# Kernel tuning notes

Hardware: AMD Instinct MI355X
Metric: run time of the kernel (lower is better)

## Reference

```python
import jax, jax.numpy as jnp
import numpy as np

J = 16384
D = 2048

def setup_inputs() -> dict:
    key = jax.random.key(0)
    embeddings = jax.random.normal(key, (J, D), dtype=jnp.float32)
    return {"embeddings": embeddings}

def reference(embeddings) -> jnp.ndarray:
    J_, d = embeddings.shape
    # position indices j=1..J, feature indices k=1..d (as in the torch loop)
    j = jnp.arange(1, J_ + 1, dtype=embeddings.dtype)  # [J]
    k = jnp.arange(1, d + 1, dtype=embeddings.dtype)   # [d]
    a = 1.0 - j / J_            # [J]
    b = 1.0 - 2.0 * j / J_      # [J]
    # L[j,k] = (1 - j/J) - (k/d)*(1 - 2j/J)
    L = a[:, None] - (k / d)[None, :] * b[:, None]  # [J, d]
    return jnp.sum(L * embeddings, axis=0)  # [d]
```

## Files before the change

### kernel.cpp

```cpp
#include <hip/hip_runtime.h>


constexpr int D_COLS = 2048;
constexpr int J_ROWS = 16384;
constexpr int T1  = 512;
constexpr int NB1 = 1024;
constexpr int RPB = J_ROWS / NB1;

__global__ __launch_bounds__(T1, 8) void pe_stage1(const float* __restrict__ E,
                                                   float* __restrict__ ws) {
    const int tid  = threadIdx.x;
    const int col0 = tid * 4;
    const int b    = blockIdx.x;
    const int row0 = b * RPB;
    const float invJ = 1.0f / (float)J_ROWS;
    const float invD = 1.0f / (float)D_COLS;
    const float c0 = (float)(col0 + 1) * invD;
    const float c1 = (float)(col0 + 2) * invD;
    const float c2 = (float)(col0 + 3) * invD;
    const float c3 = (float)(col0 + 4) * invD;

    const float* base = E + (size_t)row0 * D_COLS + col0;

    float4 acc = make_float4(0.f, 0.f, 0.f, 0.f);
    #pragma unroll 1
    for (int it = 0; it < RPB / 4; ++it) {
        const int r = it * 4;
        const float4 e0 = *reinterpret_cast<const float4*>(base + (size_t)(r + 0) * D_COLS);
        const float4 e1 = *reinterpret_cast<const float4*>(base + (size_t)(r + 1) * D_COLS);
        const float4 e2 = *reinterpret_cast<const float4*>(base + (size_t)(r + 2) * D_COLS);
        const float4 e3 = *reinterpret_cast<const float4*>(base + (size_t)(r + 3) * D_COLS);

        const float j0 = (float)(row0 + r + 1);
        const float j1 = j0 + 1.0f, j2 = j0 + 2.0f, j3 = j0 + 3.0f;
        const float a0 = fmaf(-j0, invJ, 1.0f), bb0 = fmaf(-2.f * j0, invJ, 1.0f);
        const float a1 = fmaf(-j1, invJ, 1.0f), bb1 = fmaf(-2.f * j1, invJ, 1.0f);
        const float a2 = fmaf(-j2, invJ, 1.0f), bb2 = fmaf(-2.f * j2, invJ, 1.0f);
        const float a3 = fmaf(-j3, invJ, 1.0f), bb3 = fmaf(-2.f * j3, invJ, 1.0f);

        acc.x = fmaf(fmaf(-c0, bb0, a0), e0.x, acc.x);
        acc.y = fmaf(fmaf(-c1, bb0, a0), e0.y, acc.y);
        acc.z = fmaf(fmaf(-c2, bb0, a0), e0.z, acc.z);
        acc.w = fmaf(fmaf(-c3, bb0, a0), e0.w, acc.w);
        acc.x = fmaf(fmaf(-c0, bb1, a1), e1.x, acc.x);
        acc.y = fmaf(fmaf(-c1, bb1, a1), e1.y, acc.y);
        acc.z = fmaf(fmaf(-c2, bb1, a1), e1.z, acc.z);
        acc.w = fmaf(fmaf(-c3, bb1, a1), e1.w, acc.w);
        acc.x = fmaf(fmaf(-c0, bb2, a2), e2.x, acc.x);
        acc.y = fmaf(fmaf(-c1, bb2, a2), e2.y, acc.y);
        acc.z = fmaf(fmaf(-c2, bb2, a2), e2.z, acc.z);
        acc.w = fmaf(fmaf(-c3, bb2, a2), e2.w, acc.w);
        acc.x = fmaf(fmaf(-c0, bb3, a3), e3.x, acc.x);
        acc.y = fmaf(fmaf(-c1, bb3, a3), e3.y, acc.y);
        acc.z = fmaf(fmaf(-c2, bb3, a3), e3.z, acc.z);
        acc.w = fmaf(fmaf(-c3, bb3, a3), e3.w, acc.w);
    }

    ws[(size_t)(col0 + 0) * NB1 + b] = acc.x;
    ws[(size_t)(col0 + 1) * NB1 + b] = acc.y;
    ws[(size_t)(col0 + 2) * NB1 + b] = acc.z;
    ws[(size_t)(col0 + 3) * NB1 + b] = acc.w;
}

__global__ __launch_bounds__(256) void pe_stage2(const float* __restrict__ ws,
                                                 float* __restrict__ out) {
    const int wave = threadIdx.x >> 6;
    const int lane = threadIdx.x & 63;
    const int col  = blockIdx.x * 4 + wave;
    const float4* p = reinterpret_cast<const float4*>(ws + (size_t)col * NB1);
    const float4 v0 = p[lane];
    const float4 v1 = p[lane + 64];
    const float4 v2 = p[lane + 128];
    const float4 v3 = p[lane + 192];
    float s = (((v0.x + v0.y) + (v0.z + v0.w)) + ((v1.x + v1.y) + (v1.z + v1.w)))
            + (((v2.x + v2.y) + (v2.z + v2.w)) + ((v3.x + v3.y) + (v3.z + v3.w)));
    #pragma unroll
    for (int off = 32; off > 0; off >>= 1)
        s += __shfl_down(s, off, 64);
    if (lane == 0) out[col] = s;
}

extern "C" void kernel_launch(void* const* d_in, const int* in_sizes, int n_in,
                              void* d_out, int out_size, void* d_ws, size_t ws_size,
                              hipStream_t stream) {
    const float* E = (const float*)d_in[0];
    float* out = (float*)d_out;
    float* ws = (float*)d_ws;
    (void)in_sizes; (void)n_in; (void)out_size; (void)ws_size;

    pe_stage1<<<NB1, T1, 0, stream>>>(E, ws);
    pe_stage2<<<D_COLS / 4, 256, 0, stream>>>(ws, out);
}
```

Measured before the change: 210.1 us.

## Store partials row-major with float4 and reduce in two coalesced stages

Stage 1 now writes each block's partial sums as one contiguous float4 row instead of four strided scalar stores into a column-major workspace. The final reduction is split into two kernels: one sums groups of 16 partial rows into 64 rows, and another sums those 64 rows per column. This targets the uncoalesced scattered writes in stage 1. It adds a third kernel launch and an extra workspace round trip.

Result: faster. 194.2 us (-7.6%).

```diff
diff --git a/kernel.cpp b/kernel.cpp
--- a/kernel.cpp
+++ b/kernel.cpp
@@ -6,6 +6,7 @@
 constexpr int T1  = 512;
 constexpr int NB1 = 1024;
 constexpr int RPB = J_ROWS / NB1;
+constexpr int NB2 = 64;
 
 __global__ __launch_bounds__(T1, 8) void pe_stage1(const float* __restrict__ E,
                                                    float* __restrict__ ws) {
@@ -56,28 +57,35 @@
         acc.w = fmaf(fmaf(-c3, bb3, a3), e3.w, acc.w);
     }
 
-    ws[(size_t)(col0 + 0) * NB1 + b] = acc.x;
-    ws[(size_t)(col0 + 1) * NB1 + b] = acc.y;
-    ws[(size_t)(col0 + 2) * NB1 + b] = acc.z;
-    ws[(size_t)(col0 + 3) * NB1 + b] = acc.w;
+    *reinterpret_cast<float4*>(ws + (size_t)b * D_COLS + col0) = acc;
 }
 
-__global__ __launch_bounds__(256) void pe_stage2(const float* __restrict__ ws,
-                                                 float* __restrict__ out) {
-    const int wave = threadIdx.x >> 6;
-    const int lane = threadIdx.x & 63;
-    const int col  = blockIdx.x * 4 + wave;
-    const float4* p = reinterpret_cast<const float4*>(ws + (size_t)col * NB1);
-    const float4 v0 = p[lane];
-    const float4 v1 = p[lane + 64];
-    const float4 v2 = p[lane + 128];
-    const float4 v3 = p[lane + 192];
-    float s = (((v0.x + v0.y) + (v0.z + v0.w)) + ((v1.x + v1.y) + (v1.z + v1.w)))
-            + (((v2.x + v2.y) + (v2.z + v2.w)) + ((v3.x + v3.y) + (v3.z + v3.w)));
+__global__ __launch_bounds__(T1) void pe_stage2(const float* __restrict__ ws,
+                                                float* __restrict__ ws2) {
+    const int col0 = threadIdx.x * 4;
+    const int b    = blockIdx.x;
+    const float* base = ws + (size_t)(b * (NB1 / NB2)) * D_COLS + col0;
+    float4 acc = make_float4(0.f, 0.f, 0.f, 0.f);
     #pragma unroll
-    for (int off = 32; off > 0; off >>= 1)
-        s += __shfl_down(s, off, 64);
-    if (lane == 0) out[col] = s;
+    for (int r = 0; r < NB1 / NB2; ++r) {
+        const float4 v = *reinterpret_cast<const float4*>(base + (size_t)r * D_COLS);
+        acc.x += v.x; acc.y += v.y; acc.z += v.z; acc.w += v.w;
+    }
+    *reinterpret_cast<float4*>(ws2 + (size_t)b * D_COLS + col0) = acc;
+}
+
+__global__ __launch_bounds__(T1) void pe_stage3(const float* __restrict__ ws2,
+                                                float* __restrict__ out) {
+    const int k = blockIdx.x * T1 + threadIdx.x;
+    float s0 = 0.f, s1 = 0.f, s2 = 0.f, s3 = 0.f;
+    #pragma unroll
+    for (int r = 0; r < NB2; r += 4) {
+        s0 += ws2[(size_t)(r + 0) * D_COLS + k];
+        s1 += ws2[(size_t)(r + 1) * D_COLS + k];
+        s2 += ws2[(size_t)(r + 2) * D_COLS + k];
+        s3 += ws2[(size_t)(r + 3) * D_COLS + k];
+    }
+    out[k] = (s0 + s1) + (s2 + s3);
 }
 
 extern "C" void kernel_launch(void* const* d_in, const int* in_sizes, int n_in,
@@ -85,9 +93,11 @@
                               hipStream_t stream) {
     const float* E = (const float*)d_in[0];
     float* out = (float*)d_out;
-    float* ws = (float*)d_ws;
+    float* ws  = (float*)d_ws;
+    float* ws2 = ws + (size_t)NB1 * D_COLS;
     (void)in_sizes; (void)n_in; (void)out_size; (void)ws_size;
 
     pe_stage1<<<NB1, T1, 0, stream>>>(E, ws);
-    pe_stage2<<<D_COLS / 4, 256, 0, stream>>>(ws, out);
+    pe_stage2<<<NB2, T1, 0, stream>>>(ws, ws2);
+    pe_stage3<<<D_COLS / T1, T1, 0, stream>>>(ws2, out);
 }
```
